# Kernel tuning notes

Measured on AMD Instinct MI355X. Metric: run time of the kernel, lower is better.

The kernel has to match this reference:

```python
import jax, jax.numpy as jnp
import numpy as np

B, N, D = 256, 2048, 256

def setup_inputs() -> dict:
    key = jax.random.key(0)
    k1, k2, k3, k4 = jax.random.split(key, 4)
    feature = jax.random.normal(k1, (B, N, D), dtype=jnp.float32)
    pointer_hidden_state = jax.random.normal(k2, (B, D), dtype=jnp.float32)
    # learned params (match torch.randn init)
    v = jax.random.normal(k3, (1, 1, D), dtype=jnp.float32)
    W = jax.random.normal(k4, (1, D, 2 * D), dtype=jnp.float32)
    return {"feature": feature, "pointer_hidden_state": pointer_hidden_state, "v": v, "W": W}

def reference(feature, pointer_hidden_state, v, W):
    # hidden: concat(feature, broadcast hidden state) -> [B, N, 2D]
    b, n, d = feature.shape
    h = jnp.broadcast_to(pointer_hidden_state[:, None, :], (b, n, d))
    hidden = jnp.concatenate([feature, h], axis=2)            # [B, N, 2D]
    # W @ hidden^T fused as einsum: [D, 2D] x [B, N, 2D] -> [B, N, D]
    pre = jnp.tanh(jnp.einsum('de,bne->bnd', W[0], hidden))
    # v . pre -> [B, N]
    scores = jnp.einsum('d,bnd->bn', v[0, 0], pre)
    attns = jax.nn.softmax(scores, axis=1)[:, None, :]        # [B, 1, N]
    return attns
```

## Files before the change

### kernel.cpp

```cpp
#include <hip/hip_runtime.h>
#include <hip/hip_fp16.h>

typedef _Float16 f16;
typedef _Float16 f16x4 __attribute__((ext_vector_type(4)));
typedef _Float16 f16x8 __attribute__((ext_vector_type(8)));
typedef __fp16 h16x2 __attribute__((ext_vector_type(2)));
typedef float f32x4 __attribute__((ext_vector_type(4)));

#define NCH 64
#define CHB 32768
#define PSTRIDE 524288

#define BAR()    asm volatile("s_waitcnt lgkmcnt(0)\n\ts_barrier" ::: "memory")
#define WAITV(N) asm volatile("s_waitcnt vmcnt(" #N ")" ::: "memory")

__global__ void prep_w(const float* __restrict__ W, f16* __restrict__ wbuf) {
    int idx = blockIdx.x * 256 + threadIdx.x;
    int d = idx >> 8, k = idx & 255;
    float w = W[d * 512 + k];
    int ct   = d >> 4;
    int lane = (d & 15) | (((k >> 3) & 3) << 4);
    int ks   = k >> 5;
    int j    = k & 7;
    wbuf[(((ks * 16 + ct) * 64) + lane) * 8 + j] = (f16)w;
}

__global__ void prep_c(const float* __restrict__ W, const float* __restrict__ h,
                       float* __restrict__ c) {
    __shared__ float hs[256];
    int b = blockIdx.x, d = threadIdx.x;
    hs[d] = h[b * 256 + d];
    __syncthreads();
    const float4* w4 = (const float4*)(W + d * 512 + 256);
    const float4* h4 = (const float4*)hs;
    float acc = 0.f;
#pragma unroll 8
    for (int e = 0; e < 64; ++e) {
        float4 a = w4[e], bb = h4[e];
        acc += a.x * bb.x + a.y * bb.y + a.z * bb.z + a.w * bb.w;
    }
    c[b * 256 + d] = acc;
}

__global__ __launch_bounds__(512, 2)
void main_gemm(const float* __restrict__ feat, const f16* __restrict__ wbuf,
               const float* __restrict__ cb, const float* __restrict__ vvec,
               float* __restrict__ psc) {
    __shared__ __align__(16) char rawb[2 * CHB];
    __shared__ __align__(16) char plnb[2 * CHB];

    const int tid = threadIdx.x;
    const int w = tid >> 6;
    const int l = tid & 63;
    const int g = l >> 4;
    const int lr = l & 15;
    const int rh = w >> 2;
    const int cg = w & 3;
    const int b = blockIdx.x;

    f16x8 wf[4][8];
    {
        const f16x8* wp = (const f16x8*)wbuf;
#pragma unroll
        for (int ct = 0; ct < 4; ++ct) {
            int ctg = cg * 4 + ct;
#pragma unroll
            for (int ks = 0; ks < 8; ++ks)
                wf[ct][ks] = wp[(ks * 16 + ctg) * 64 + l];
        }
    }
    float c_[4], v_[4];
#pragma unroll
    for (int ct = 0; ct < 4; ++ct) {
        c_[ct] = cb[b * 256 + (cg * 4 + ct) * 16 + lr];
        v_[ct] = vvec[(cg * 4 + ct) * 16 + lr];
    }

    const char* tbb = (const char*)(feat + (size_t)b * 2048 * 256);

#define ISSUE(u)                                                                   \
    {                                                                              \
        const char* nb = tbb + (size_t)(u) * CHB;                                  \
        char* Q = rawb + ((u) & 1) * CHB;                                          \
        _Pragma("unroll")                                                          \
        for (int i = 0; i < 4; ++i)                                                \
            __builtin_amdgcn_global_load_lds(                                      \
                (const __attribute__((address_space(1))) void*)(nb + i * 8192 + tid * 16), \
                (__attribute__((address_space(3))) void*)(Q + i * 8192 + tid * 16),\
                16, 0, 0);                                                         \
    }

    const int ck0 = (tid & 63) * 4;
    int cvt_off[4];
#pragma unroll
    for (int r = 0; r < 4; ++r) {
        int row = r * 8 + w;
        cvt_off[r] = (((row * 512 + (ck0 & ~7) * 2) ^ ((row & 7) << 4)) +
                      ((ck0 & 4) << 1));
    }

#define CVT(u)                                                                     \
    {                                                                              \
        const char* rp = rawb + ((u) & 1) * CHB;                                   \
        char* hp = plnb + ((u) & 1) * CHB;                                         \
        _Pragma("unroll")                                                          \
        for (int r = 0; r < 4; ++r) {                                              \
            f32x4 x = *(const f32x4*)(rp + r * 8192 + tid * 16);                   \
            h16x2 h01 = __builtin_amdgcn_cvt_pkrtz(x[0], x[1]);                    \
            h16x2 h23 = __builtin_amdgcn_cvt_pkrtz(x[2], x[3]);                    \
            h16x2 l01 = __builtin_amdgcn_cvt_pkrtz(x[0] - (float)h01[0],           \
                                                   x[1] - (float)h01[1]);          \
            h16x2 l23 = __builtin_amdgcn_cvt_pkrtz(x[2] - (float)h23[0],           \
                                                   x[3] - (float)h23[1]);          \
            f16x4 hv = {(f16)(float)h01[0], (f16)(float)h01[1],                    \
                        (f16)(float)h23[0], (f16)(float)h23[1]};                   \
            f16x4 lv = {(f16)(float)l01[0], (f16)(float)l01[1],                    \
                        (f16)(float)l23[0], (f16)(float)l23[1]};                   \
            *(f16x4*)(hp + cvt_off[r]) = hv;                                       \
            *(f16x4*)(hp + 16384 + cvt_off[r]) = lv;                               \
        }                                                                          \
    }

    const int arow = rh * 16 + lr;
    const int aswz = (arow & 7) << 4;

    ISSUE(0); ISSUE(1);
    WAITV(4);
    CVT(0);

    for (int t = 0; t < NCH; ++t) {
        BAR();
        if (t + 2 < NCH) ISSUE(t + 2);

        const char* hp = plnb + (t & 1) * CHB;
        f32x4 acc[4] = {};
#pragma unroll
        for (int ks = 0; ks < 8; ++ks) {
            int ao = (arow * 512 + ks * 64 + g * 16) ^ aswz;
            f16x8 ahi = *(const f16x8*)(hp + ao);
            f16x8 alo = *(const f16x8*)(hp + 16384 + ao);
            acc[0] = __builtin_amdgcn_mfma_f32_16x16x32_f16(ahi, wf[0][ks], acc[0], 0, 0, 0);
            acc[1] = __builtin_amdgcn_mfma_f32_16x16x32_f16(ahi, wf[1][ks], acc[1], 0, 0, 0);
            acc[2] = __builtin_amdgcn_mfma_f32_16x16x32_f16(ahi, wf[2][ks], acc[2], 0, 0, 0);
            acc[3] = __builtin_amdgcn_mfma_f32_16x16x32_f16(ahi, wf[3][ks], acc[3], 0, 0, 0);
            acc[0] = __builtin_amdgcn_mfma_f32_16x16x32_f16(alo, wf[0][ks], acc[0], 0, 0, 0);
            acc[1] = __builtin_amdgcn_mfma_f32_16x16x32_f16(alo, wf[1][ks], acc[1], 0, 0, 0);
            acc[2] = __builtin_amdgcn_mfma_f32_16x16x32_f16(alo, wf[2][ks], acc[2], 0, 0, 0);
            acc[3] = __builtin_amdgcn_mfma_f32_16x16x32_f16(alo, wf[3][ks], acc[3], 0, 0, 0);
        }

        float s[4];
#pragma unroll
        for (int r = 0; r < 4; ++r) {
            float a = 0.f;
#pragma unroll
            for (int ct = 0; ct < 4; ++ct) {
                float x = acc[ct][r] + c_[ct];
                float tnh = 1.f - __fdividef(2.f, __expf(2.f * x) + 1.f);
                a += v_[ct] * tnh;
            }
            s[r] = a;
        }
#pragma unroll
        for (int m = 1; m < 16; m <<= 1) {
            s[0] += __shfl_xor(s[0], m, 64);
            s[1] += __shfl_xor(s[1], m, 64);
            s[2] += __shfl_xor(s[2], m, 64);
            s[3] += __shfl_xor(s[3], m, 64);
        }

        if (t < NCH - 2)      WAITV(4);
        else if (t == NCH - 2) WAITV(0);
        if (t + 1 < NCH) CVT(t + 1);

        if (lr == 0) {
            size_t rowg = (size_t)b * 2048 + t * 32 + rh * 16 + g * 4;
            float4 o = {s[0], s[1], s[2], s[3]};
            *(float4*)(psc + (size_t)cg * PSTRIDE + rowg) = o;
        }
    }
#undef ISSUE
#undef CVT
}

__global__ void softmax_k(const float* __restrict__ psc, float* __restrict__ out) {
    __shared__ float red[16];
    int b = blockIdx.x, tid = threadIdx.x;
    float sc[8];
    float m = -3.4e38f;
#pragma unroll
    for (int q = 0; q < 8; ++q) {
        size_t row = (size_t)b * 2048 + q * 256 + tid;
        sc[q] = (psc[row] + psc[PSTRIDE + row]) +
                (psc[2 * PSTRIDE + row] + psc[3 * PSTRIDE + row]);
        m = fmaxf(m, sc[q]);
    }
#pragma unroll
    for (int d = 1; d < 64; d <<= 1) m = fmaxf(m, __shfl_xor(m, d, 64));
    if ((tid & 63) == 0) red[tid >> 6] = m;
    __syncthreads();
    m = fmaxf(fmaxf(red[0], red[1]), fmaxf(red[2], red[3]));
    float e[8], sum = 0.f;
#pragma unroll
    for (int q = 0; q < 8; ++q) { e[q] = __expf(sc[q] - m); sum += e[q]; }
#pragma unroll
    for (int d = 1; d < 64; d <<= 1) sum += __shfl_xor(sum, d, 64);
    if ((tid & 63) == 0) red[8 + (tid >> 6)] = sum;
    __syncthreads();
    sum = (red[8] + red[9]) + (red[10] + red[11]);
    float inv = __fdividef(1.f, sum);
#pragma unroll
    for (int q = 0; q < 8; ++q)
        out[(size_t)b * 2048 + q * 256 + tid] = e[q] * inv;
}

extern "C" void kernel_launch(void* const* d_in, const int* in_sizes, int n_in,
                              void* d_out, int out_size, void* d_ws, size_t ws_size,
                              hipStream_t stream) {
    const float* feat = (const float*)d_in[0];
    const float* h    = (const float*)d_in[1];
    const float* v    = (const float*)d_in[2];
    const float* W    = (const float*)d_in[3];
    float* out = (float*)d_out;

    f16*   wbuf = (f16*)d_ws;
    float* cbuf = (float*)((char*)d_ws + 131072);
    float* psc  = (float*)((char*)d_ws + 524288);

    prep_w<<<256, 256, 0, stream>>>(W, wbuf);
    prep_c<<<256, 256, 0, stream>>>(W, h, cbuf);
    main_gemm<<<256, 512, 0, stream>>>(feat, wbuf, cbuf, v, psc);
    softmax_k<<<256, 256, 0, stream>>>(psc, out);
}
```

Before: 209.5 us.

## Interleave chunk loads and conversion with MFMA phases using barriers and setprio

Splits each chunk's MFMA loop into four phases. Each phase issues one slice of the next-next chunk's global-to-LDS load, converts one slice of the next chunk to hi/lo fp16, then runs its MFMAs at raised wave priority between barriers. The goal is to overlap memory and conversion with matrix work at a finer grain, in the style of a ping-pong schedule across waves. The cost is many more barriers per chunk and finer vmcnt waits, and the first and last iterations are peeled to keep the wait counts correct.

```diff
diff --git a/kernel.cpp b/kernel.cpp
--- a/kernel.cpp
+++ b/kernel.cpp
@@ -11,8 +11,9 @@
 #define CHB 32768
 #define PSTRIDE 524288
 
-#define BAR()    asm volatile("s_waitcnt lgkmcnt(0)\n\ts_barrier" ::: "memory")
-#define WAITV(N) asm volatile("s_waitcnt vmcnt(" #N ")" ::: "memory")
+#define BAR()     asm volatile("s_waitcnt lgkmcnt(0)\n\ts_barrier" ::: "memory")
+#define WAITV_(N) asm volatile("s_waitcnt vmcnt(" #N ")" ::: "memory")
+#define WAITV(N)  WAITV_(N)
 
 __global__ void prep_w(const float* __restrict__ W, f16* __restrict__ wbuf) {
     int idx = blockIdx.x * 256 + threadIdx.x;
@@ -78,16 +79,14 @@
 
     const char* tbb = (const char*)(feat + (size_t)b * 2048 * 256);
 
-#define ISSUE(u)                                                                   \
+#define ISSUE1(u, i)                                                               \
     {                                                                              \
         const char* nb = tbb + (size_t)(u) * CHB;                                  \
         char* Q = rawb + ((u) & 1) * CHB;                                          \
-        _Pragma("unroll")                                                          \
-        for (int i = 0; i < 4; ++i)                                                \
-            __builtin_amdgcn_global_load_lds(                                      \
-                (const __attribute__((address_space(1))) void*)(nb + i * 8192 + tid * 16), \
-                (__attribute__((address_space(3))) void*)(Q + i * 8192 + tid * 16),\
-                16, 0, 0);                                                         \
+        __builtin_amdgcn_global_load_lds(                                          \
+            (const __attribute__((address_space(1))) void*)(nb + (i) * 8192 + tid * 16), \
+            (__attribute__((address_space(3))) void*)(Q + (i) * 8192 + tid * 16),  \
+            16, 0, 0);                                                             \
     }
 
     const int ck0 = (tid & 63) * 4;
@@ -99,88 +98,130 @@
                       ((ck0 & 4) << 1));
     }
 
-#define CVT(u)                                                                     \
+#define CVT1(u, r)                                                                 \
     {                                                                              \
         const char* rp = rawb + ((u) & 1) * CHB;                                   \
-        char* hp = plnb + ((u) & 1) * CHB;                                         \
+        char* hq = plnb + ((u) & 1) * CHB;                                         \
+        f32x4 x = *(const f32x4*)(rp + (r) * 8192 + tid * 16);                     \
+        h16x2 h01 = __builtin_amdgcn_cvt_pkrtz(x[0], x[1]);                        \
+        h16x2 h23 = __builtin_amdgcn_cvt_pkrtz(x[2], x[3]);                        \
+        h16x2 l01 = __builtin_amdgcn_cvt_pkrtz(x[0] - (float)h01[0],               \
+                                               x[1] - (float)h01[1]);              \
+        h16x2 l23 = __builtin_amdgcn_cvt_pkrtz(x[2] - (float)h23[0],               \
+                                               x[3] - (float)h23[1]);              \
+        f16x4 hv = {(f16)(float)h01[0], (f16)(float)h01[1],                        \
+                    (f16)(float)h23[0], (f16)(float)h23[1]};                       \
+        f16x4 lv = {(f16)(float)l01[0], (f16)(float)l01[1],                        \
+                    (f16)(float)l23[0], (f16)(float)l23[1]};                       \
+        *(f16x4*)(hq + cvt_off[r]) = hv;                                           \
+        *(f16x4*)(hq + 16384 + cvt_off[r]) = lv;                                   \
+    }
+
+    const int arow = rh * 16 + lr;
+    const int aswz = (arow & 7) << 4;
+
+#define PHASE(P, T, WS, DOISS, DOCVT)                                              \
+    {                                                                              \
+        const char* hp = plnb + ((T) & 1) * CHB;                                   \
+        int ao0 = (arow * 512 + (2 * (P)) * 64 + g * 16) ^ aswz;                   \
+        int ao1 = (arow * 512 + (2 * (P) + 1) * 64 + g * 16) ^ aswz;               \
+        f16x8 ah0 = *(const f16x8*)(hp + ao0);                                     \
+        f16x8 al0 = *(const f16x8*)(hp + 16384 + ao0);                             \
+        f16x8 ah1 = *(const f16x8*)(hp + ao1);                                     \
+        f16x8 al1 = *(const f16x8*)(hp + 16384 + ao1);                             \
+        if (DOISS) ISSUE1((T) + 2, P);                                             \
+        WS;                                                                        \
+        if (DOCVT) CVT1((T) + 1, P);                                               \
+        __builtin_amdgcn_s_barrier();                                              \
+        __builtin_amdgcn_s_setprio(1);                                             \
+        acc[0] = __builtin_amdgcn_mfma_f32_16x16x32_f16(ah0, wf[0][2*(P)], acc[0], 0, 0, 0); \
+        acc[1] = __builtin_amdgcn_mfma_f32_16x16x32_f16(ah0, wf[1][2*(P)], acc[1], 0, 0, 0); \
+        acc[2] = __builtin_amdgcn_mfma_f32_16x16x32_f16(ah0, wf[2][2*(P)], acc[2], 0, 0, 0); \
+        acc[3] = __builtin_amdgcn_mfma_f32_16x16x32_f16(ah0, wf[3][2*(P)], acc[3], 0, 0, 0); \
+        acc[0] = __builtin_amdgcn_mfma_f32_16x16x32_f16(al0, wf[0][2*(P)], acc[0], 0, 0, 0); \
+        acc[1] = __builtin_amdgcn_mfma_f32_16x16x32_f16(al0, wf[1][2*(P)], acc[1], 0, 0, 0); \
+        acc[2] = __builtin_amdgcn_mfma_f32_16x16x32_f16(al0, wf[2][2*(P)], acc[2], 0, 0, 0); \
+        acc[3] = __builtin_amdgcn_mfma_f32_16x16x32_f16(al0, wf[3][2*(P)], acc[3], 0, 0, 0); \
+        acc[0] = __builtin_amdgcn_mfma_f32_16x16x32_f16(ah1, wf[0][2*(P)+1], acc[0], 0, 0, 0); \
+        acc[1] = __builtin_amdgcn_mfma_f32_16x16x32_f16(ah1, wf[1][2*(P)+1], acc[1], 0, 0, 0); \
+        acc[2] = __builtin_amdgcn_mfma_f32_16x16x32_f16(ah1, wf[2][2*(P)+1], acc[2], 0, 0, 0); \
+        acc[3] = __builtin_amdgcn_mfma_f32_16x16x32_f16(ah1, wf[3][2*(P)+1], acc[3], 0, 0, 0); \
+        acc[0] = __builtin_amdgcn_mfma_f32_16x16x32_f16(al1, wf[0][2*(P)+1], acc[0], 0, 0, 0); \
+        acc[1] = __builtin_amdgcn_mfma_f32_16x16x32_f16(al1, wf[1][2*(P)+1], acc[1], 0, 0, 0); \
+        acc[2] = __builtin_amdgcn_mfma_f32_16x16x32_f16(al1, wf[2][2*(P)+1], acc[2], 0, 0, 0); \
+        acc[3] = __builtin_amdgcn_mfma_f32_16x16x32_f16(al1, wf[3][2*(P)+1], acc[3], 0, 0, 0); \
+        __builtin_amdgcn_s_setprio(0);                                             \
+        __builtin_amdgcn_s_barrier();                                              \
+    }
+
+#define EPI(T)                                                                     \
+    {                                                                              \
+        float s[4];                                                                \
         _Pragma("unroll")                                                          \
         for (int r = 0; r < 4; ++r) {                                              \
-            f32x4 x = *(const f32x4*)(rp + r * 8192 + tid * 16);                   \
-            h16x2 h01 = __builtin_amdgcn_cvt_pkrtz(x[0], x[1]);                    \
-            h16x2 h23 = __builtin_amdgcn_cvt_pkrtz(x[2], x[3]);                    \
-            h16x2 l01 = __builtin_amdgcn_cvt_pkrtz(x[0] - (float)h01[0],           \
-                                                   x[1] - (float)h01[1]);          \
-            h16x2 l23 = __builtin_amdgcn_cvt_pkrtz(x[2] - (float)h23[0],           \
-                                                   x[3] - (float)h23[1]);          \
-            f16x4 hv = {(f16)(float)h01[0], (f16)(float)h01[1],                    \
-                        (f16)(float)h23[0], (f16)(float)h23[1]};                   \
-            f16x4 lv = {(f16)(float)l01[0], (f16)(float)l01[1],                    \
-                        (f16)(float)l23[0], (f16)(float)l23[1]};                   \
-            *(f16x4*)(hp + cvt_off[r]) = hv;                                       \
-            *(f16x4*)(hp + 16384 + cvt_off[r]) = lv;                               \
+            float a = 0.f;                                                         \
+            _Pragma("unroll")                                                      \
+            for (int ct = 0; ct < 4; ++ct) {                                       \
+                float x = acc[ct][r] + c_[ct];                                     \
+                float tnh = 1.f - __fdividef(2.f, __expf(2.f * x) + 1.f);          \
+                a += v_[ct] * tnh;                                                 \
+            }                                                                      \
+            s[r] = a;                                                              \
         }                                                                          \
-    }
-
-    const int arow = rh * 16 + lr;
-    const int aswz = (arow & 7) << 4;
-
-    ISSUE(0); ISSUE(1);
+        _Pragma("unroll")                                                          \
+        for (int m = 1; m < 16; m <<= 1) {                                         \
+            s[0] += __shfl_xor(s[0], m, 64);                                       \
+            s[1] += __shfl_xor(s[1], m, 64);                                       \
+            s[2] += __shfl_xor(s[2], m, 64);                                       \
+            s[3] += __shfl_xor(s[3], m, 64);                                       \
+        }                                                                          \
+        if (lr == 0) {                                                             \
+            size_t rowg = (size_t)b * 2048 + (T) * 32 + rh * 16 + g * 4;           \
+            float4 o = {s[0], s[1], s[2], s[3]};                                   \
+            *(float4*)(psc + (size_t)cg * PSTRIDE + rowg) = o;                     \
+        }                                                                          \
+        BAR();                                                                     \
+    }
+
+#pragma unroll
+    for (int i = 0; i < 4; ++i) ISSUE1(0, i);
+#pragma unroll
+    for (int i = 0; i < 4; ++i) ISSUE1(1, i);
     WAITV(4);
-    CVT(0);
-
-    for (int t = 0; t < NCH; ++t) {
-        BAR();
-        if (t + 2 < NCH) ISSUE(t + 2);
-
-        const char* hp = plnb + (t & 1) * CHB;
+#pragma unroll
+    for (int r = 0; r < 4; ++r) CVT1(0, r);
+    BAR();
+
+    for (int t = 0; t < NCH - 2; ++t) {
         f32x4 acc[4] = {};
-#pragma unroll
-        for (int ks = 0; ks < 8; ++ks) {
-            int ao = (arow * 512 + ks * 64 + g * 16) ^ aswz;
-            f16x8 ahi = *(const f16x8*)(hp + ao);
-            f16x8 alo = *(const f16x8*)(hp + 16384 + ao);
-            acc[0] = __builtin_amdgcn_mfma_f32_16x16x32_f16(ahi, wf[0][ks], acc[0], 0, 0, 0);
-            acc[1] = __builtin_amdgcn_mfma_f32_16x16x32_f16(ahi, wf[1][ks], acc[1], 0, 0, 0);
-            acc[2] = __builtin_amdgcn_mfma_f32_16x16x32_f16(ahi, wf[2][ks], acc[2], 0, 0, 0);
-            acc[3] = __builtin_amdgcn_mfma_f32_16x16x32_f16(ahi, wf[3][ks], acc[3], 0, 0, 0);
-            acc[0] = __builtin_amdgcn_mfma_f32_16x16x32_f16(alo, wf[0][ks], acc[0], 0, 0, 0);
-            acc[1] = __builtin_amdgcn_mfma_f32_16x16x32_f16(alo, wf[1][ks], acc[1], 0, 0, 0);
-            acc[2] = __builtin_amdgcn_mfma_f32_16x16x32_f16(alo, wf[2][ks], acc[2], 0, 0, 0);
-            acc[3] = __builtin_amdgcn_mfma_f32_16x16x32_f16(alo, wf[3][ks], acc[3], 0, 0, 0);
-        }
-
-        float s[4];
-#pragma unroll
-        for (int r = 0; r < 4; ++r) {
-            float a = 0.f;
-#pragma unroll
-            for (int ct = 0; ct < 4; ++ct) {
-                float x = acc[ct][r] + c_[ct];
-                float tnh = 1.f - __fdividef(2.f, __expf(2.f * x) + 1.f);
-                a += v_[ct] * tnh;
-            }
-            s[r] = a;
-        }
-#pragma unroll
-        for (int m = 1; m < 16; m <<= 1) {
-            s[0] += __shfl_xor(s[0], m, 64);
-            s[1] += __shfl_xor(s[1], m, 64);
-            s[2] += __shfl_xor(s[2], m, 64);
-            s[3] += __shfl_xor(s[3], m, 64);
-        }
-
-        if (t < NCH - 2)      WAITV(4);
-        else if (t == NCH - 2) WAITV(0);
-        if (t + 1 < NCH) CVT(t + 1);
-
-        if (lr == 0) {
-            size_t rowg = (size_t)b * 2048 + t * 32 + rh * 16 + g * 4;
-            float4 o = {s[0], s[1], s[2], s[3]};
-            *(float4*)(psc + (size_t)cg * PSTRIDE + rowg) = o;
-        }
-    }
-#undef ISSUE
-#undef CVT
+        PHASE(0, t, WAITV(4), 1, 1)
+        PHASE(1, t, WAITV(4), 1, 1)
+        PHASE(2, t, WAITV(4), 1, 1)
+        PHASE(3, t, WAITV(4), 1, 1)
+        EPI(t)
+    }
+    {
+        const int t = NCH - 2;
+        f32x4 acc[4] = {};
+        PHASE(0, t, WAITV(3), 0, 1)
+        PHASE(1, t, WAITV(2), 0, 1)
+        PHASE(2, t, WAITV(1), 0, 1)
+        PHASE(3, t, WAITV(0), 0, 1)
+        EPI(t)
+    }
+    {
+        const int t = NCH - 1;
+        f32x4 acc[4] = {};
+        PHASE(0, t, ((void)0), 0, 0)
+        PHASE(1, t, ((void)0), 0, 0)
+        PHASE(2, t, ((void)0), 0, 0)
+        PHASE(3, t, ((void)0), 0, 0)
+        EPI(t)
+    }
+#undef ISSUE1
+#undef CVT1
+#undef PHASE
+#undef EPI
 }
 
 __global__ void softmax_k(const float* __restrict__ psc, float* __restrict__ out) {
```

Result: slower. 260.7 us (+24.4%).

## Split each batch row across two 256-thread blocks of main GEMM

Applied to the files above, without the earlier changes.

The main GEMM kernel now launches two 256-thread blocks per batch instead of one 512-thread block. Each block handles half of the N rows in 16-row chunks, and the LDS staging buffers shrink to half size. Each wave now owns all 16 rows of a chunk and a 64-column slice of D. The intent is to make the two co-resident blocks per CU synchronise independently, so barrier stalls overlap better with the streaming feature loads. In exchange, the W fragments are loaded twice per batch, chunks are smaller, and the final vmcnt wait is relaxed to 1.

```diff
diff --git a/kernel.cpp b/kernel.cpp
--- a/kernel.cpp
+++ b/kernel.cpp
@@ -8,11 +8,12 @@
 typedef float f32x4 __attribute__((ext_vector_type(4)));
 
 #define NCH 64
-#define CHB 32768
+#define CHB 16384
 #define PSTRIDE 524288
 
-#define BAR()    asm volatile("s_waitcnt lgkmcnt(0)\n\ts_barrier" ::: "memory")
-#define WAITV(N) asm volatile("s_waitcnt vmcnt(" #N ")" ::: "memory")
+#define BAR()     asm volatile("s_waitcnt lgkmcnt(0)\n\ts_barrier" ::: "memory")
+#define WAITV_(N) asm volatile("s_waitcnt vmcnt(" #N ")" ::: "memory")
+#define WAITV(N)  WAITV_(N)
 
 __global__ void prep_w(const float* __restrict__ W, f16* __restrict__ wbuf) {
     int idx = blockIdx.x * 256 + threadIdx.x;
@@ -42,7 +43,7 @@
     c[b * 256 + d] = acc;
 }
 
-__global__ __launch_bounds__(512, 2)
+__global__ __launch_bounds__(256, 2)
 void main_gemm(const float* __restrict__ feat, const f16* __restrict__ wbuf,
                const float* __restrict__ cb, const float* __restrict__ vvec,
                float* __restrict__ psc) {
@@ -54,16 +55,15 @@
     const int l = tid & 63;
     const int g = l >> 4;
     const int lr = l & 15;
-    const int rh = w >> 2;
-    const int cg = w & 3;
-    const int b = blockIdx.x;
+    const int b = blockIdx.x >> 1;
+    const int half = blockIdx.x & 1;
 
     f16x8 wf[4][8];
     {
         const f16x8* wp = (const f16x8*)wbuf;
 #pragma unroll
         for (int ct = 0; ct < 4; ++ct) {
-            int ctg = cg * 4 + ct;
+            int ctg = w * 4 + ct;
 #pragma unroll
             for (int ks = 0; ks < 8; ++ks)
                 wf[ct][ks] = wp[(ks * 16 + ctg) * 64 + l];
@@ -72,11 +72,11 @@
     float c_[4], v_[4];
 #pragma unroll
     for (int ct = 0; ct < 4; ++ct) {
-        c_[ct] = cb[b * 256 + (cg * 4 + ct) * 16 + lr];
-        v_[ct] = vvec[(cg * 4 + ct) * 16 + lr];
-    }
-
-    const char* tbb = (const char*)(feat + (size_t)b * 2048 * 256);
+        c_[ct] = cb[b * 256 + (w * 4 + ct) * 16 + lr];
+        v_[ct] = vvec[(w * 4 + ct) * 16 + lr];
+    }
+
+    const char* tbb = (const char*)(feat + ((size_t)b * 2048 + half * 1024) * 256);
 
 #define ISSUE(u)                                                                   \
     {                                                                              \
@@ -85,8 +85,8 @@
         _Pragma("unroll")                                                          \
         for (int i = 0; i < 4; ++i)                                                \
             __builtin_amdgcn_global_load_lds(                                      \
-                (const __attribute__((address_space(1))) void*)(nb + i * 8192 + tid * 16), \
-                (__attribute__((address_space(3))) void*)(Q + i * 8192 + tid * 16),\
+                (const __attribute__((address_space(1))) void*)(nb + i * 4096 + tid * 16), \
+                (__attribute__((address_space(3))) void*)(Q + i * 4096 + tid * 16),\
                 16, 0, 0);                                                         \
     }
 
@@ -94,7 +94,7 @@
     int cvt_off[4];
 #pragma unroll
     for (int r = 0; r < 4; ++r) {
-        int row = r * 8 + w;
+        int row = r * 4 + (tid >> 6);
         cvt_off[r] = (((row * 512 + (ck0 & ~7) * 2) ^ ((row & 7) << 4)) +
                       ((ck0 & 4) << 1));
     }
@@ -102,10 +102,10 @@
 #define CVT(u)                                                                     \
     {                                                                              \
         const char* rp = rawb + ((u) & 1) * CHB;                                   \
-        char* hp = plnb + ((u) & 1) * CHB;                                         \
+        char* hq = plnb + ((u) & 1) * CHB;                                         \
         _Pragma("unroll")                                                          \
         for (int r = 0; r < 4; ++r) {                                              \
-            f32x4 x = *(const f32x4*)(rp + r * 8192 + tid * 16);                   \
+            f32x4 x = *(const f32x4*)(rp + r * 4096 + tid * 16);                   \
             h16x2 h01 = __builtin_amdgcn_cvt_pkrtz(x[0], x[1]);                    \
             h16x2 h23 = __builtin_amdgcn_cvt_pkrtz(x[2], x[3]);                    \
             h16x2 l01 = __builtin_amdgcn_cvt_pkrtz(x[0] - (float)h01[0],           \
@@ -116,13 +116,12 @@
                         (f16)(float)h23[0], (f16)(float)h23[1]};                   \
             f16x4 lv = {(f16)(float)l01[0], (f16)(float)l01[1],                    \
                         (f16)(float)l23[0], (f16)(float)l23[1]};                   \
-            *(f16x4*)(hp + cvt_off[r]) = hv;                                       \
-            *(f16x4*)(hp + 16384 + cvt_off[r]) = lv;                               \
+            *(f16x4*)(hq + cvt_off[r]) = hv;                                       \
+            *(f16x4*)(hq + 8192 + cvt_off[r]) = lv;                                \
         }                                                                          \
     }
 
-    const int arow = rh * 16 + lr;
-    const int aswz = (arow & 7) << 4;
+    const int aswz = (lr & 7) << 4;
 
     ISSUE(0); ISSUE(1);
     WAITV(4);
@@ -136,9 +135,9 @@
         f32x4 acc[4] = {};
 #pragma unroll
         for (int ks = 0; ks < 8; ++ks) {
-            int ao = (arow * 512 + ks * 64 + g * 16) ^ aswz;
+            int ao = (lr * 512 + ks * 64 + g * 16) ^ aswz;
             f16x8 ahi = *(const f16x8*)(hp + ao);
-            f16x8 alo = *(const f16x8*)(hp + 16384 + ao);
+            f16x8 alo = *(const f16x8*)(hp + 8192 + ao);
             acc[0] = __builtin_amdgcn_mfma_f32_16x16x32_f16(ahi, wf[0][ks], acc[0], 0, 0, 0);
             acc[1] = __builtin_amdgcn_mfma_f32_16x16x32_f16(ahi, wf[1][ks], acc[1], 0, 0, 0);
             acc[2] = __builtin_amdgcn_mfma_f32_16x16x32_f16(ahi, wf[2][ks], acc[2], 0, 0, 0);
@@ -170,13 +169,13 @@
         }
 
         if (t < NCH - 2)      WAITV(4);
-        else if (t == NCH - 2) WAITV(0);
+        else if (t == NCH - 2) WAITV(1);
         if (t + 1 < NCH) CVT(t + 1);
 
         if (lr == 0) {
-            size_t rowg = (size_t)b * 2048 + t * 32 + rh * 16 + g * 4;
+            size_t rowg = (size_t)b * 2048 + half * 1024 + t * 16 + g * 4;
             float4 o = {s[0], s[1], s[2], s[3]};
-            *(float4*)(psc + (size_t)cg * PSTRIDE + rowg) = o;
+            *(float4*)(psc + (size_t)w * PSTRIDE + rowg) = o;
         }
     }
 #undef ISSUE
@@ -229,6 +228,6 @@
 
     prep_w<<<256, 256, 0, stream>>>(W, wbuf);
     prep_c<<<256, 256, 0, stream>>>(W, h, cbuf);
-    main_gemm<<<256, 512, 0, stream>>>(feat, wbuf, cbuf, v, psc);
+    main_gemm<<<512, 256, 0, stream>>>(feat, wbuf, cbuf, v, psc);
     softmax_k<<<256, 256, 0, stream>>>(psc, out);
 }
```

New measurement: 214.9 us. 2.6% more time.
